# Kernel optimization log

Hardware: AMD Instinct MI355X
Metric: run time of the kernel (lower is better)

Reference implementation:

```python
import jax, jax.numpy as jnp
import numpy as np

H = 128        # hidden_channels
R = 32         # num_rbf
L = 2          # num_layers
CUTOFF = 4.5   # cutoff_upper (cutoff_lower = 0)
N_ATOMS = 2048
N_EDGES = 32768


def _tensor_norm(t):
    # Frobenius norm squared over the trailing 3x3 -> [N, H]
    return jnp.sum(t * t, axis=(-2, -1))


def _decompose(t):
    # Split into isotropic (I), antisymmetric (A), traceless symmetric (S) parts.
    eye = jnp.eye(3, dtype=t.dtype)
    I = (jnp.trace(t, axis1=-2, axis2=-1) / 3.0)[..., None, None] * eye
    A = 0.5 * (t - jnp.swapaxes(t, -2, -1))
    S = 0.5 * (t + jnp.swapaxes(t, -2, -1)) - I
    return I, A, S


def _chan_mix(T, W):
    # torch nn.Linear(H, H, bias=False) applied on the channel axis of [N,H,3,3]
    return jnp.einsum('nhij,gh->ngij', T, W)


def _interaction(X, edge_index, edge_weight, edge_attr, q,
                 W1, b1, W2, b2, W3, b3, Wt):
    N = X.shape[0]
    src, dst = edge_index[0], edge_index[1]
    # cosine cutoff (cutoff_lower = 0)
    C = 0.5 * (jnp.cos(edge_weight * (jnp.pi / CUTOFF)) + 1.0)
    C = C * (edge_weight < CUTOFF).astype(C.dtype)
    # edge scalar MLP: R -> H -> 2H -> 3H, silu
    ea = jax.nn.silu(edge_attr @ W1.T + b1)
    ea = jax.nn.silu(ea @ W2.T + b2)
    ea = jax.nn.silu(ea @ W3.T + b3)
    ea = (ea * C[:, None]).reshape(-1, H, 3)       # [E, H, 3]
    # normalize node tensors
    X = X / (_tensor_norm(X) + 1.0)[..., None, None]
    I, A, S = _decompose(X)
    I = _chan_mix(I, Wt[0])
    A = _chan_mix(A, Wt[1])
    S = _chan_mix(S, Wt[2])
    Y = I + A + S
    # per-edge tensor messages (Im + Am + Sm fused before the scatter)
    msg = (ea[:, :, 0, None, None] * I[dst]
           + ea[:, :, 1, None, None] * A[dst]
           + ea[:, :, 2, None, None] * S[dst])   # [E, H, 3, 3]
    M = jax.ops.segment_sum(msg, src, num_segments=N)
    # O(3) group: symmetrized tensor product, scaled by charge factor
    AB = jnp.matmul(M, Y) + jnp.matmul(Y, M)
    I, A, S = _decompose((1.0 + 0.1 * q[:, None, None, None]) * AB)
    normp1 = (_tensor_norm(I + A + S) + 1.0)[..., None, None]
    I, A, S = I / normp1, A / normp1, S / normp1
    I = _chan_mix(I, Wt[3])
    A = _chan_mix(A, Wt[4])
    S = _chan_mix(S, Wt[5])
    dX = I + A + S
    return X + dX + (1.0 + 0.1 * q[:, None, None, None]) * jnp.matmul(dX, dX)


def setup_inputs() -> dict:
    key = jax.random.key(0)
    ks = jax.random.split(key, 10)
    N, E = N_ATOMS, N_EDGES
    X = jax.random.normal(ks[0], (N, H, 3, 3), jnp.float32)
    edge_index = jax.random.randint(ks[1], (2, E), 0, N, jnp.int32)
    edge_weight = jax.random.uniform(ks[2], (E,), jnp.float32, 0.1, CUTOFF)
    edge_attr = jax.random.normal(ks[3], (E, R), jnp.float32)
    q = jax.random.normal(ks[4], (N,), jnp.float32) * 0.1
    s = 0.05
    Ws1 = jax.random.normal(ks[5], (L, H, R), jnp.float32) * s
    bs1 = jnp.zeros((L, H), jnp.float32)
    Ws2 = jax.random.normal(ks[6], (L, 2 * H, H), jnp.float32) * s
    bs2 = jnp.zeros((L, 2 * H), jnp.float32)
    Ws3 = jax.random.normal(ks[7], (L, 3 * H, 2 * H), jnp.float32) * s
    bs3 = jnp.zeros((L, 3 * H), jnp.float32)
    Wt = jax.random.normal(ks[8], (L, 6, H, H), jnp.float32) * s
    return dict(X=X, edge_attr=edge_attr, edge_weight=edge_weight, q=q,
                Ws1=Ws1, bs1=bs1, Ws2=Ws2, bs2=bs2, Ws3=Ws3, bs3=bs3,
                Wt=Wt, edge_index=edge_index)


def reference(X, edge_attr, edge_weight, q, Ws1, bs1, Ws2, bs2, Ws3, bs3, Wt, edge_index):
    for l in range(L):
        X = _interaction(X, edge_index, edge_weight, edge_attr, q,
                         Ws1[l], bs1[l], Ws2[l], bs2[l], Ws3[l], bs3[l], Wt[l])
    return X
```

## Files before the change

kernel.cpp:

```cpp
#include <hip/hip_runtime.h>
#include <hip/hip_bf16.h>
#include <math.h>

#define H 128
#define R 32
#define NATOMS 2048
#define NEDGES 32768
#define NH (NATOMS * H)
#define NP 1152
#define CUTOFF_F 4.5f
#define PI_OVER_CUTOFF 0.6981317007977318f

typedef __bf16 bf16x8 __attribute__((ext_vector_type(8)));
typedef float f32x4 __attribute__((ext_vector_type(4)));
typedef short short8 __attribute__((ext_vector_type(8)));
typedef unsigned short u16x4 __attribute__((ext_vector_type(4)));

#define BAR_LGKM() do { \
    asm volatile("s_waitcnt lgkmcnt(0)" ::: "memory"); \
    __builtin_amdgcn_s_barrier(); \
    asm volatile("" ::: "memory"); \
} while (0)

__device__ __forceinline__ float silu_f(float x) {
    return x / (1.f + __expf(-x));
}
__device__ __forceinline__ float b2f(unsigned short u) {
    return __uint_as_float(((unsigned)u) << 16);
}
__device__ __forceinline__ unsigned short f2b(float f) {
    __hip_bfloat16 h = __float2bfloat16(f);
    return __builtin_bit_cast(unsigned short, h);
}

__device__ __forceinline__ void build_full(const float d[9], float m[9]) {
    float i0 = d[0], a01 = d[1], a02 = d[2], a12 = d[3];
    float s00 = d[4], s01 = d[5], s02 = d[6], s11 = d[7], s12 = d[8];
    float s22 = -(s00 + s11);
    m[0] = i0 + s00;  m[1] = a01 + s01;  m[2] = a02 + s02;
    m[3] = s01 - a01; m[4] = i0 + s11;   m[5] = a12 + s12;
    m[6] = s02 - a02; m[7] = s12 - a12;  m[8] = i0 + s22;
}

#define C0 (NEDGES * R)
#define C1 (2 * H * R)
#define C2 (2 * 2 * H * H)
#define C3 (2 * 3 * H * 2 * H)
#define C4 (2 * 6 * H * H)
#define C5 2048
#define CAST_TOTAL (C0 + C1 + C2 + C3 + C4 + C5 + NH)
__global__ __launch_bounds__(256) void k_cast_all(
        const float* __restrict__ ea, const float* __restrict__ w1,
        const float* __restrict__ w2, const float* __restrict__ w3,
        const float* __restrict__ wt,
        __hip_bfloat16* __restrict__ oea, __hip_bfloat16* __restrict__ ow1,
        __hip_bfloat16* __restrict__ ow2, __hip_bfloat16* __restrict__ ow3,
        __hip_bfloat16* __restrict__ owt, int* __restrict__ cnt,
        const float* __restrict__ X, float* __restrict__ Xn,
        __hip_bfloat16* __restrict__ Db) {
    int i = blockIdx.x * 256 + threadIdx.x;
    if (i < C0) { oea[i] = __float2bfloat16(ea[i]); return; }
    i -= C0;
    if (i < C1) { ow1[i] = __float2bfloat16(w1[i]); return; }
    i -= C1;
    if (i < C2) { ow2[i] = __float2bfloat16(w2[i]); return; }
    i -= C2;
    if (i < C3) { ow3[i] = __float2bfloat16(w3[i]); return; }
    i -= C3;
    if (i < C4) { owt[i] = __float2bfloat16(wt[i]); return; }
    i -= C4;
    if (i < C5) { cnt[i] = 0; return; }
    i -= C5;
    if (i < NH) {
        const float* x = X + (size_t)i * 9;
        float v[9];
        float ss = 0.f;
#pragma unroll
        for (int j = 0; j < 9; j++) { v[j] = x[j]; ss += v[j] * v[j]; }
        float inv = 1.f / (ss + 1.f);
#pragma unroll
        for (int j = 0; j < 9; j++) { v[j] *= inv; Xn[(size_t)i * 9 + j] = v[j]; }
        float i0 = (v[0] + v[4] + v[8]) * (1.f / 3.f);
        unsigned short* D = (unsigned short*)Db + (size_t)(i >> 7) * NP + (i & 127);
        D[0 * H] = f2b(i0);
        D[1 * H] = f2b(0.5f * (v[1] - v[3]));
        D[2 * H] = f2b(0.5f * (v[2] - v[6]));
        D[3 * H] = f2b(0.5f * (v[5] - v[7]));
        D[4 * H] = f2b(v[0] - i0);
        D[5 * H] = f2b(0.5f * (v[1] + v[3]));
        D[6 * H] = f2b(0.5f * (v[2] + v[6]));
        D[7 * H] = f2b(v[4] - i0);
        D[8 * H] = f2b(0.5f * (v[5] + v[7]));
    }
}

struct TGm {
    static constexpr int BKm = 64;
    static constexpr int RB  = 128;
    static constexpr int SWZ = 7;
    static constexpr int NIT = 2;
    static constexpr int ABYTES = 128 * RB;
    static constexpr int BBYTES = 64 * RB;
    static constexpr int AISS = ABYTES / 4096;
    static constexpr int BISS = BBYTES / 4096;
    static constexpr int LDSB = ABYTES + BBYTES;
};

__device__ __forceinline__ void tile_gemm_mix(
        const __hip_bfloat16* __restrict__ A, int strideA,
        const __hip_bfloat16* __restrict__ W,
        int m0, int n0, char* lds, f32x4 acc[4][2]) {
    using T = TGm;
    const int t = threadIdx.x;
    const int lane = t & 63;
    const int w = t >> 6;

    auto stage = [&](int b, int it) {
        const int k0 = it * T::BKm;
        char* As = lds + b * T::LDSB;
        char* Bs = As + T::ABYTES;
#pragma unroll
        for (int i = 0; i < T::AISS; i++) {
            int base = (w * T::AISS + i) * 1024;
            int lin = base + lane * 16;
            int row = lin / T::RB;
            int slot = (lin % T::RB) >> 4;
            int sl = slot ^ (row & T::SWZ);
            const char* src = (const char*)(A + (size_t)(m0 + row) * strideA + k0) + sl * 16;
            __builtin_amdgcn_global_load_lds(
                (const __attribute__((address_space(1))) void*)src,
                (__attribute__((address_space(3))) void*)(As + base), 16, 0, 0);
        }
#pragma unroll
        for (int i = 0; i < T::BISS; i++) {
            int base = (w * T::BISS + i) * 1024;
            int lin = base + lane * 16;
            int row = lin / T::RB;
            int slot = (lin % T::RB) >> 4;
            int sl = slot ^ (row & T::SWZ);
            const char* src = (const char*)(W + (size_t)(n0 + row) * H + k0) + sl * 16;
            __builtin_amdgcn_global_load_lds(
                (const __attribute__((address_space(1))) void*)src,
                (__attribute__((address_space(3))) void*)(Bs + base), 16, 0, 0);
        }
    };

    auto compute = [&](int b) {
        const char* As = lds + b * T::LDSB;
        const char* Bs = As + T::ABYTES;
        const int wm = (w & 1) * 64;
        const int wn = (w >> 1) * 32;
        const int rA = wm + (lane & 15);
        const int rB = wn + (lane & 15);
        const int c = lane >> 4;
#pragma unroll
        for (int kk = 0; kk < T::BKm / 32; kk++) {
            bf16x8 av[4], bv[2];
#pragma unroll
            for (int mf = 0; mf < 4; mf++) {
                int row = rA + mf * 16;
                int sp = (kk * 4 + c) ^ (row & T::SWZ);
                av[mf] = __builtin_bit_cast(bf16x8,
                    *(const short8*)(As + row * T::RB + sp * 16));
            }
#pragma unroll
            for (int nf = 0; nf < 2; nf++) {
                int row = rB + nf * 16;
                int sp = (kk * 4 + c) ^ (row & T::SWZ);
                bv[nf] = __builtin_bit_cast(bf16x8,
                    *(const short8*)(Bs + row * T::RB + sp * 16));
            }
#pragma unroll
            for (int mf = 0; mf < 4; mf++)
#pragma unroll
                for (int nf = 0; nf < 2; nf++)
                    acc[mf][nf] = __builtin_amdgcn_mfma_f32_16x16x32_bf16(
                        av[mf], bv[nf], acc[mf][nf], 0, 0, 0);
        }
    };

    stage(0, 0);
    asm volatile("s_waitcnt vmcnt(0)" ::: "memory");
    __syncthreads();
    for (int it = 0; it < T::NIT; it++) {
        int b = it & 1;
        if (it + 1 < T::NIT) stage(b ^ 1, it + 1);
        compute(b);
        asm volatile("s_waitcnt vmcnt(0)" ::: "memory");
        __syncthreads();
    }
}

__global__ __launch_bounds__(256) void k_mix(
        const __hip_bfloat16* __restrict__ Db, const __hip_bfloat16* __restrict__ Wtb,
        __hip_bfloat16* __restrict__ Outp, int partOff) {
    __shared__ char lds[2 * TGm::LDSB];
    int c = blockIdx.z;
    int part = (c == 0) ? 0 : ((c < 4) ? 1 : 2);
    const __hip_bfloat16* A = Db + (size_t)c * H;
    const __hip_bfloat16* W = Wtb + (size_t)(partOff + part) * H * H;
    unsigned short* Out = (unsigned short*)Outp + (size_t)c * H;
    const int lane = threadIdx.x & 63;
    const int w = threadIdx.x >> 6;
    const int wm = (w & 1) * 64, wn = (w >> 1) * 32;
    const int m0 = blockIdx.x * 128, n0 = blockIdx.y * 64;
    f32x4 acc[4][2] = {};
    tile_gemm_mix(A, NP, W, m0, n0, lds, acc);
#pragma unroll
    for (int mf = 0; mf < 4; mf++)
#pragma unroll
        for (int r = 0; r < 4; r++) {
            int row = m0 + wm + mf * 16 + (lane >> 4) * 4 + r;
#pragma unroll
            for (int nf = 0; nf < 2; nf++) {
                int col = n0 + wn + nf * 16 + (lane & 15);
                Out[(size_t)row * NP + col] = f2b(acc[mf][nf][r]);
            }
        }
}

#define ETILE 64
#define PAD0 40
#define PAD1 136
#define PAD2 264
#define SA2_B (ETILE * PAD2 * 2)
#define SA1_B (ETILE * PAD1 * 2)
#define SEA_OFF SA1_B

__global__ __launch_bounds__(512, 4) void k_mlp_fused(
        const __hip_bfloat16* __restrict__ eaB,
        const __hip_bfloat16* __restrict__ W1b, const __hip_bfloat16* __restrict__ W2b,
        const __hip_bfloat16* __restrict__ W3b,
        const float* __restrict__ bs1, const float* __restrict__ bs2,
        const float* __restrict__ bs3, const float* __restrict__ ew,
        __hip_bfloat16* __restrict__ ea3g) {
    const int l = blockIdx.z;
    const unsigned short* W1 = (const unsigned short*)W1b + (size_t)l * (H * R);
    const unsigned short* W2 = (const unsigned short*)W2b + (size_t)l * (2 * H * H);
    const unsigned short* W3 = (const unsigned short*)W3b + (size_t)l * (3 * H * 2 * H);
    const float* b1 = bs1 + (size_t)l * H;
    const float* b2 = bs2 + (size_t)l * 2 * H;
    const float* b3 = bs3 + (size_t)l * 3 * H;
    unsigned short* outp = (unsigned short*)ea3g + (size_t)l * NEDGES * 384;
    const int e0 = blockIdx.x * ETILE;

    __shared__ char smem[SA2_B + ETILE * 4 + 16];
    unsigned short* sA2 = (unsigned short*)smem;
    unsigned short* sA1 = (unsigned short*)smem;
    unsigned short* sEA = (unsigned short*)(smem + SEA_OFF);
    float* sEW = (float*)(smem + SA2_B);

    const int t = threadIdx.x;
    const int lane = t & 63;
    const int w = t >> 6;
    const int q = lane >> 4;
    const int li = lane & 15;

    const int cbase1 = w * 16;
    const int cbase2 = w * 32;
    const int cbase3 = w * 48;

    bf16x8 av1 = __builtin_bit_cast(bf16x8,
        *(const short8*)(W1 + (size_t)(cbase1 + li) * R + q * 8));
    f32x4 bb1 = *(const f32x4*)&b1[cbase1 + q * 4];

    {
        if (t < 256) {
            int row = t >> 2, c8 = t & 3;
            *(uint4*)(sEA + row * PAD0 + c8 * 8) =
                *(const uint4*)((const unsigned short*)eaB + (size_t)(e0 + row) * R + c8 * 8);
        }
        if (t < ETILE) sEW[t] = ew[e0 + t];
    }
    BAR_LGKM();

    f32x4 acc1[4] = {};
#pragma unroll
    for (int ef = 0; ef < 4; ef++) {
        bf16x8 bv = __builtin_bit_cast(bf16x8,
            *(const short8*)(sEA + (ef * 16 + li) * PAD0 + q * 8));
        acc1[ef] = __builtin_amdgcn_mfma_f32_16x16x32_bf16(av1, bv, acc1[ef], 0, 0, 0);
    }

    bf16x8 a2[4][2];
#pragma unroll
    for (int ks = 0; ks < 4; ks++)
#pragma unroll
        for (int mf = 0; mf < 2; mf++)
            a2[ks][mf] = __builtin_bit_cast(bf16x8,
                *(const short8*)(W2 + (size_t)(cbase2 + mf * 16 + li) * H
                                 + ks * 32 + q * 8));
    f32x4 bb2[2];
#pragma unroll
    for (int mf = 0; mf < 2; mf++)
        bb2[mf] = *(const f32x4*)&b2[cbase2 + mf * 16 + q * 4];

#pragma unroll
    for (int ef = 0; ef < 4; ef++) {
        u16x4 o;
#pragma unroll
        for (int r = 0; r < 4; r++) o[r] = f2b(silu_f(acc1[ef][r] + bb1[r]));
        *(u16x4*)(sA1 + (ef * 16 + li) * PAD1 + cbase1 + q * 4) = o;
    }
    BAR_LGKM();

    f32x4 acc2[2][4] = {};
#pragma unroll
    for (int ks = 0; ks < 4; ks++) {
        bf16x8 bv[4];
#pragma unroll
        for (int ef = 0; ef < 4; ef++)
            bv[ef] = __builtin_bit_cast(bf16x8,
                *(const short8*)(sA1 + (ef * 16 + li) * PAD1 + ks * 32 + q * 8));
        __builtin_amdgcn_s_setprio(1);
#pragma unroll
        for (int mf = 0; mf < 2; mf++)
#pragma unroll
            for (int ef = 0; ef < 4; ef++)
                acc2[mf][ef] = __builtin_amdgcn_mfma_f32_16x16x32_bf16(
                    a2[ks][mf], bv[ef], acc2[mf][ef], 0, 0, 0);
        __builtin_amdgcn_s_setprio(0);
    }

    bf16x8 a3[3][3];
#pragma unroll
    for (int pk = 0; pk < 3; pk++)
#pragma unroll
        for (int mf = 0; mf < 3; mf++)
            a3[pk][mf] = __builtin_bit_cast(bf16x8,
                *(const short8*)(W3 + (size_t)(cbase3 + mf * 16 + li) * (2 * H)
                                 + pk * 32 + q * 8));

    BAR_LGKM();
#pragma unroll
    for (int mf = 0; mf < 2; mf++)
#pragma unroll
        for (int ef = 0; ef < 4; ef++) {
            u16x4 o;
#pragma unroll
            for (int r = 0; r < 4; r++)
                o[r] = f2b(silu_f(acc2[mf][ef][r] + bb2[mf][r]));
            *(u16x4*)(sA2 + (ef * 16 + li) * PAD2 + cbase2 + mf * 16 + q * 4) = o;
        }
    BAR_LGKM();

    f32x4 acc3[3][4] = {};
#pragma unroll
    for (int ks = 0; ks < 8; ks++) {
        const int slot = ks % 3;
        bf16x8 bv[4];
#pragma unroll
        for (int ef = 0; ef < 4; ef++)
            bv[ef] = __builtin_bit_cast(bf16x8,
                *(const short8*)(sA2 + (ef * 16 + li) * PAD2 + ks * 32 + q * 8));
        __builtin_amdgcn_s_setprio(1);
#pragma unroll
        for (int mf = 0; mf < 3; mf++)
#pragma unroll
            for (int ef = 0; ef < 4; ef++)
                acc3[mf][ef] = __builtin_amdgcn_mfma_f32_16x16x32_bf16(
                    a3[slot][mf], bv[ef], acc3[mf][ef], 0, 0, 0);
        __builtin_amdgcn_s_setprio(0);
        if (ks + 3 < 8) {
#pragma unroll
            for (int mf = 0; mf < 3; mf++)
                a3[slot][mf] = __builtin_bit_cast(bf16x8,
                    *(const short8*)(W3 + (size_t)(cbase3 + mf * 16 + li) * (2 * H)
                                     + (ks + 3) * 32 + q * 8));
        }
    }
    f32x4 bb3[3];
#pragma unroll
    for (int mf = 0; mf < 3; mf++)
        bb3[mf] = *(const f32x4*)&b3[cbase3 + mf * 16 + q * 4];
#pragma unroll
    for (int ef = 0; ef < 4; ef++) {
        int edge = ef * 16 + li;
        float wv = sEW[edge];
        float cs = (wv < CUTOFF_F) ? 0.5f * (__cosf(wv * PI_OVER_CUTOFF) + 1.f) : 0.f;
#pragma unroll
        for (int mf = 0; mf < 3; mf++) {
            u16x4 o;
#pragma unroll
            for (int r = 0; r < 4; r++)
                o[r] = f2b(silu_f(acc3[mf][ef][r] + bb3[mf][r]) * cs);
            *(u16x4*)(outp + (size_t)(e0 + edge) * 384 + cbase3 + mf * 16 + q * 4) = o;
        }
    }
}

__global__ __launch_bounds__(256) void k_hist(
        const int* __restrict__ eidx, int* __restrict__ cnt) {
    int e = blockIdx.x * 256 + threadIdx.x;
    if (e < NEDGES) atomicAdd(&cnt[eidx[e]], 1);
}

__global__ __launch_bounds__(256) void k_scan(
        const int* __restrict__ cnt, int* __restrict__ rowstart,
        int* __restrict__ cursor) {
    __shared__ int partial[256];
    int t = threadIdx.x;
    int loc[8];
    int run = 0;
#pragma unroll
    for (int j = 0; j < 8; j++) {
        int v = cnt[t * 8 + j];
        loc[j] = run; run += v;
    }
    partial[t] = run;
    __syncthreads();
    if (t == 0) {
        int acc = 0;
        for (int i = 0; i < 256; i++) { int v = partial[i]; partial[i] = acc; acc += v; }
        rowstart[2048] = acc;
    }
    __syncthreads();
    int base = partial[t];
#pragma unroll
    for (int j = 0; j < 8; j++) {
        rowstart[t * 8 + j] = base + loc[j];
        cursor[t * 8 + j] = base + loc[j];
    }
}

__global__ __launch_bounds__(256) void k_fill(
        const int* __restrict__ eidx, int* __restrict__ cursor,
        int* __restrict__ elist) {
    int e = blockIdx.x * 256 + threadIdx.x;
    if (e >= NEDGES) return;
    int src = eidx[e];
    int pos = atomicAdd(&cursor[src], 1);
    elist[pos] = e;
}

__global__ __launch_bounds__(256) void k_gather_ab(
        const __hip_bfloat16* __restrict__ ea ,
        const int* __restrict__ eidx,
        const int* __restrict__ rowstart, const int* __restrict__ elist,
        const __hip_bfloat16* __restrict__ Yb, const float* __restrict__ q,
        __hip_bfloat16* __restrict__ Tb) {
    int gid = blockIdx.x * 256 + threadIdx.x;
    int n = gid >> 7;
    int t7 = gid & 127;
    int hp = t7 >> 1;
    int half = t7 & 1;
    int h0 = hp << 1;
    int beg = rowstart[n], end = rowstart[n + 1];
    const unsigned short* Y = (const unsigned short*)Yb;

    int hcol = h0 + half;
    const unsigned short* ypn = Y + (size_t)n * NP + hcol;
    float yd[9];
#pragma unroll
    for (int c = 0; c < 9; c++) yd[c] = b2f(ypn[(size_t)c * H]);

    float acc[9][2];
#pragma unroll
    for (int c = 0; c < 9; c++) { acc[c][0] = 0.f; acc[c][1] = 0.f; }

    int idx = beg + half;
    int e = 0, dst = 0;
    if (idx < end) { e = elist[idx]; dst = eidx[NEDGES + e]; }
    while (idx < end) {
        int nidx = idx + 2;
        int ne = e, ndst = dst;
        if (nidx < end) { ne = elist[nidx]; ndst = eidx[NEDGES + ne]; }
        const unsigned short* eap = (const unsigned short*)ea + (size_t)e * 384 + h0 * 3;
        unsigned u0 = *(const unsigned*)(eap);
        unsigned u1 = *(const unsigned*)(eap + 2);
        unsigned u2 = *(const unsigned*)(eap + 4);
        float w0a = b2f(u0 & 0xffff), w1a = b2f(u0 >> 16);
        float w2a = b2f(u1 & 0xffff), w0b = b2f(u1 >> 16);
        float w1b = b2f(u2 & 0xffff), w2b = b2f(u2 >> 16);
        const unsigned short* yp = Y + (size_t)dst * NP + h0;
        ushort2 y;
        y = *(const ushort2*)(yp + 0 * H); acc[0][0] += w0a * b2f(y.x); acc[0][1] += w0b * b2f(y.y);
        y = *(const ushort2*)(yp + 1 * H); acc[1][0] += w1a * b2f(y.x); acc[1][1] += w1b * b2f(y.y);
        y = *(const ushort2*)(yp + 2 * H); acc[2][0] += w1a * b2f(y.x); acc[2][1] += w1b * b2f(y.y);
        y = *(const ushort2*)(yp + 3 * H); acc[3][0] += w1a * b2f(y.x); acc[3][1] += w1b * b2f(y.y);
#pragma unroll
        for (int c = 4; c < 9; c++) {
            y = *(const ushort2*)(yp + c * H);
            acc[c][0] += w2a * b2f(y.x); acc[c][1] += w2b * b2f(y.y);
        }
        idx = nidx; e = ne; dst = ndst;
    }
#pragma unroll
    for (int c = 0; c < 9; c++) {
        acc[c][0] += __shfl_xor(acc[c][0], 1);
        acc[c][1] += __shfl_xor(acc[c][1], 1);
    }
    float scale = 1.f + 0.1f * q[n];
    float md[9];
#pragma unroll
    for (int c = 0; c < 9; c++) md[c] = acc[c][half];
    float m[9], yf[9];
    build_full(md, m);
    build_full(yd, yf);
    float ab[9];
#pragma unroll
    for (int ii = 0; ii < 3; ii++)
#pragma unroll
        for (int jj = 0; jj < 3; jj++) {
            float s = 0.f;
#pragma unroll
            for (int kk = 0; kk < 3; kk++)
                s += m[ii * 3 + kk] * yf[kk * 3 + jj] + yf[ii * 3 + kk] * m[kk * 3 + jj];
            ab[ii * 3 + jj] = s;
        }
    float nrm = 0.f;
#pragma unroll
    for (int j = 0; j < 9; j++) { ab[j] *= scale; nrm += ab[j] * ab[j]; }
    float inv = 1.f / (nrm + 1.f);
    float tr3 = (ab[0] + ab[4] + ab[8]) * (1.f / 3.f);
    unsigned short* T = (unsigned short*)Tb + (size_t)n * NP + hcol;
    T[0 * H] = f2b(tr3 * inv);
    T[1 * H] = f2b(0.5f * (ab[1] - ab[3]) * inv);
    T[2 * H] = f2b(0.5f * (ab[2] - ab[6]) * inv);
    T[3 * H] = f2b(0.5f * (ab[5] - ab[7]) * inv);
    T[4 * H] = f2b((ab[0] - tr3) * inv);
    T[5 * H] = f2b(0.5f * (ab[1] + ab[3]) * inv);
    T[6 * H] = f2b(0.5f * (ab[2] + ab[6]) * inv);
    T[7 * H] = f2b((ab[4] - tr3) * inv);
    T[8 * H] = f2b(0.5f * (ab[5] + ab[7]) * inv);
}

template <bool PREP>
__global__ __launch_bounds__(256) void k_final(
        const __hip_bfloat16* __restrict__ dXb, const float* __restrict__ Xn,
        const float* __restrict__ q, float* __restrict__ Xout,
        float* __restrict__ XnW, __hip_bfloat16* __restrict__ Db) {
    int i = blockIdx.x * 256 + threadIdx.x;
    if (i >= NH) return;
    const unsigned short* dX = (const unsigned short*)dXb + (size_t)(i >> 7) * NP + (i & 127);
    float dd[9];
#pragma unroll
    for (int c = 0; c < 9; c++) dd[c] = b2f(dX[(size_t)c * H]);
    float dx[9];
    build_full(dd, dx);
    float scale = 1.f + 0.1f * q[i >> 7];
    float out[9];
#pragma unroll
    for (int ii = 0; ii < 3; ii++)
#pragma unroll
        for (int jj = 0; jj < 3; jj++) {
            float s = 0.f;
#pragma unroll
            for (int kk = 0; kk < 3; kk++)
                s += dx[ii * 3 + kk] * dx[kk * 3 + jj];
            out[ii * 3 + jj] = Xn[(size_t)i * 9 + ii * 3 + jj] + dx[ii * 3 + jj] + scale * s;
        }
#pragma unroll
    for (int j = 0; j < 9; j++) Xout[(size_t)i * 9 + j] = out[j];
    if (PREP) {
        float ss = 0.f;
#pragma unroll
        for (int j = 0; j < 9; j++) ss += out[j] * out[j];
        float inv = 1.f / (ss + 1.f);
        float v[9];
#pragma unroll
        for (int j = 0; j < 9; j++) { v[j] = out[j] * inv; XnW[(size_t)i * 9 + j] = v[j]; }
        float i0 = (v[0] + v[4] + v[8]) * (1.f / 3.f);
        unsigned short* D = (unsigned short*)Db + (size_t)(i >> 7) * NP + (i & 127);
        D[0 * H] = f2b(i0);
        D[1 * H] = f2b(0.5f * (v[1] - v[3]));
        D[2 * H] = f2b(0.5f * (v[2] - v[6]));
        D[3 * H] = f2b(0.5f * (v[5] - v[7]));
        D[4 * H] = f2b(v[0] - i0);
        D[5 * H] = f2b(0.5f * (v[1] + v[3]));
        D[6 * H] = f2b(0.5f * (v[2] + v[6]));
        D[7 * H] = f2b(v[4] - i0);
        D[8 * H] = f2b(0.5f * (v[5] + v[7]));
    }
}

extern "C" void kernel_launch(void* const* d_in, const int* in_sizes, int n_in,
                              void* d_out, int out_size, void* d_ws, size_t ws_size,
                              hipStream_t stream) {
    const float* X          = (const float*)d_in[0];
    const float* edge_attr  = (const float*)d_in[1];
    const float* edge_weight= (const float*)d_in[2];
    const float* q          = (const float*)d_in[3];
    const float* Ws1        = (const float*)d_in[4];
    const float* bs1        = (const float*)d_in[5];
    const float* Ws2        = (const float*)d_in[6];
    const float* bs2        = (const float*)d_in[7];
    const float* Ws3        = (const float*)d_in[8];
    const float* bs3        = (const float*)d_in[9];
    const float* Wt         = (const float*)d_in[10];
    const int*   eidx       = (const int*)d_in[11];
    float* Xout = (float*)d_out;

    char* p = (char*)d_ws;
    auto alloc = [&](size_t bytes) -> char* {
        char* r = p; p += (bytes + 255) & ~(size_t)255; return r;
    };
    size_t nodeBytes = (size_t)NH * 9 * sizeof(float);
    float* Xn   = (float*)alloc(nodeBytes);
    __hip_bfloat16* Db = (__hip_bfloat16*)alloc((size_t)NH * 9 * 2);
    __hip_bfloat16* Yb = (__hip_bfloat16*)alloc((size_t)NH * 9 * 2);
    __hip_bfloat16* eaB = (__hip_bfloat16*)alloc((size_t)C0 * 2);
    __hip_bfloat16* W1b = (__hip_bfloat16*)alloc((size_t)C1 * 2);
    __hip_bfloat16* W2b = (__hip_bfloat16*)alloc((size_t)C2 * 2);
    __hip_bfloat16* W3b = (__hip_bfloat16*)alloc((size_t)C3 * 2);
    __hip_bfloat16* Wtb = (__hip_bfloat16*)alloc((size_t)C4 * 2);
    __hip_bfloat16* ea3g = (__hip_bfloat16*)alloc((size_t)2 * NEDGES * 384 * 2);
    int* cnt      = (int*)alloc(2048 * 4);
    int* rowstart = (int*)alloc(2049 * 4);
    int* cursor   = (int*)alloc(2048 * 4);
    int* elist    = (int*)alloc(NEDGES * 4);

    k_cast_all<<<(CAST_TOTAL + 255) / 256, 256, 0, stream>>>(
        edge_attr, Ws1, Ws2, Ws3, Wt, eaB, W1b, W2b, W3b, Wtb, cnt,
        X, Xn, Db);

    k_hist<<<NEDGES / 256, 256, 0, stream>>>(eidx, cnt);
    k_scan<<<1, 256, 0, stream>>>(cnt, rowstart, cursor);
    k_fill<<<NEDGES / 256, 256, 0, stream>>>(eidx, cursor, elist);

    k_mlp_fused<<<dim3(NEDGES / ETILE, 1, 2), 512, 0, stream>>>(
        eaB, W1b, W2b, W3b, bs1, bs2, bs3, edge_weight, ea3g);

    for (int l = 0; l < 2; l++) {
        const __hip_bfloat16* Wtl = Wtb + (size_t)l * 6 * H * H;
        const __hip_bfloat16* ea3 = ea3g + (size_t)l * NEDGES * 384;

        k_mix<<<dim3(NATOMS / 128, 2, 9), 256, 0, stream>>>(Db, Wtl, Yb, 0);
        k_gather_ab<<<NH / 256, 256, 0, stream>>>(
            ea3, eidx, rowstart, elist, Yb, q, Db);
        k_mix<<<dim3(NATOMS / 128, 2, 9), 256, 0, stream>>>(Db, Wtl, Yb, 3);
        if (l == 0)
            k_final<true><<<NH / 256, 256, 0, stream>>>(Yb, Xn, q, Xout, Xn, Db);
        else
            k_final<false><<<NH / 256, 256, 0, stream>>>(Yb, Xn, q, Xout, nullptr, nullptr);
    }
}
```

Before: 158.4 us.

## Interleave Y components per channel pair for vector gathers, use four lanes per pair

The first k_mix now writes Y in a layout where the 9 components of each channel pair sit contiguously (24 halves, padded row stride). k_gather_ab can then fetch a neighbour's data with two 16-byte loads and one 4-byte load instead of nine scattered 4-byte loads. It also splits each channel pair's edge list across four lanes instead of two, doubling the thread count and reducing with an extra shuffle stage. The s_setprio hints are removed from the edge MLP kernel. The padded layout spends more memory, and half of the lanes sit idle in the epilogue.

```diff
diff --git a/kernel.cpp b/kernel.cpp
--- a/kernel.cpp
+++ b/kernel.cpp
@@ -8,6 +8,7 @@
 #define NEDGES 32768
 #define NH (NATOMS * H)
 #define NP 1152
+#define NPY 1536
 #define CUTOFF_F 4.5f
 #define PI_OVER_CUTOFF 0.6981317007977318f
 
@@ -27,6 +28,12 @@
 }
 __device__ __forceinline__ float b2f(unsigned short u) {
     return __uint_as_float(((unsigned)u) << 16);
+}
+__device__ __forceinline__ float b2f_lo(unsigned u) {
+    return __uint_as_float(u << 16);
+}
+__device__ __forceinline__ float b2f_hi(unsigned u) {
+    return __uint_as_float(u & 0xffff0000u);
 }
 __device__ __forceinline__ unsigned short f2b(float f) {
     __hip_bfloat16 h = __float2bfloat16(f);
@@ -191,6 +198,7 @@
     }
 }
 
+template <int LAYOUT>
 __global__ __launch_bounds__(256) void k_mix(
         const __hip_bfloat16* __restrict__ Db, const __hip_bfloat16* __restrict__ Wtb,
         __hip_bfloat16* __restrict__ Outp, int partOff) {
@@ -199,7 +207,7 @@
     int part = (c == 0) ? 0 : ((c < 4) ? 1 : 2);
     const __hip_bfloat16* A = Db + (size_t)c * H;
     const __hip_bfloat16* W = Wtb + (size_t)(partOff + part) * H * H;
-    unsigned short* Out = (unsigned short*)Outp + (size_t)c * H;
+    unsigned short* O = (unsigned short*)Outp;
     const int lane = threadIdx.x & 63;
     const int w = threadIdx.x >> 6;
     const int wm = (w & 1) * 64, wn = (w >> 1) * 32;
@@ -214,7 +222,11 @@
 #pragma unroll
             for (int nf = 0; nf < 2; nf++) {
                 int col = n0 + wn + nf * 16 + (lane & 15);
-                Out[(size_t)row * NP + col] = f2b(acc[mf][nf][r]);
+                if (LAYOUT == 0)
+                    O[(size_t)row * NP + (size_t)c * H + col] = f2b(acc[mf][nf][r]);
+                else
+                    O[(size_t)row * NPY + (col >> 1) * 24 + c * 2 + (col & 1)] =
+                        f2b(acc[mf][nf][r]);
             }
         }
 }
@@ -312,14 +324,12 @@
         for (int ef = 0; ef < 4; ef++)
             bv[ef] = __builtin_bit_cast(bf16x8,
                 *(const short8*)(sA1 + (ef * 16 + li) * PAD1 + ks * 32 + q * 8));
-        __builtin_amdgcn_s_setprio(1);
 #pragma unroll
         for (int mf = 0; mf < 2; mf++)
 #pragma unroll
             for (int ef = 0; ef < 4; ef++)
                 acc2[mf][ef] = __builtin_amdgcn_mfma_f32_16x16x32_bf16(
                     a2[ks][mf], bv[ef], acc2[mf][ef], 0, 0, 0);
-        __builtin_amdgcn_s_setprio(0);
     }
 
     bf16x8 a3[3][3];
@@ -353,14 +363,12 @@
         for (int ef = 0; ef < 4; ef++)
             bv[ef] = __builtin_bit_cast(bf16x8,
                 *(const short8*)(sA2 + (ef * 16 + li) * PAD2 + ks * 32 + q * 8));
-        __builtin_amdgcn_s_setprio(1);
 #pragma unroll
         for (int mf = 0; mf < 3; mf++)
 #pragma unroll
             for (int ef = 0; ef < 4; ef++)
                 acc3[mf][ef] = __builtin_amdgcn_mfma_f32_16x16x32_bf16(
                     a3[slot][mf], bv[ef], acc3[mf][ef], 0, 0, 0);
-        __builtin_amdgcn_s_setprio(0);
         if (ks + 3 < 8) {
 #pragma unroll
             for (int mf = 0; mf < 3; mf++)
@@ -437,63 +445,68 @@
         const __hip_bfloat16* __restrict__ ea ,
         const int* __restrict__ eidx,
         const int* __restrict__ rowstart, const int* __restrict__ elist,
-        const __hip_bfloat16* __restrict__ Yb, const float* __restrict__ q,
-        __hip_bfloat16* __restrict__ Tb) {
+        const __hip_bfloat16* __restrict__ Yb ,
+        const float* __restrict__ q,
+        __hip_bfloat16* __restrict__ Tb ) {
     int gid = blockIdx.x * 256 + threadIdx.x;
-    int n = gid >> 7;
-    int t7 = gid & 127;
-    int hp = t7 >> 1;
-    int half = t7 & 1;
+    int n = gid >> 8;
+    int t8 = gid & 255;
+    int hp = t8 >> 2;
+    int quarter = t8 & 3;
     int h0 = hp << 1;
     int beg = rowstart[n], end = rowstart[n + 1];
     const unsigned short* Y = (const unsigned short*)Yb;
 
-    int hcol = h0 + half;
-    const unsigned short* ypn = Y + (size_t)n * NP + hcol;
-    float yd[9];
-#pragma unroll
-    for (int c = 0; c < 9; c++) yd[c] = b2f(ypn[(size_t)c * H]);
-
     float acc[9][2];
 #pragma unroll
     for (int c = 0; c < 9; c++) { acc[c][0] = 0.f; acc[c][1] = 0.f; }
 
-    int idx = beg + half;
+    int idx = beg + quarter;
     int e = 0, dst = 0;
     if (idx < end) { e = elist[idx]; dst = eidx[NEDGES + e]; }
     while (idx < end) {
-        int nidx = idx + 2;
+        int nidx = idx + 4;
         int ne = e, ndst = dst;
         if (nidx < end) { ne = elist[nidx]; ndst = eidx[NEDGES + ne]; }
         const unsigned short* eap = (const unsigned short*)ea + (size_t)e * 384 + h0 * 3;
         unsigned u0 = *(const unsigned*)(eap);
         unsigned u1 = *(const unsigned*)(eap + 2);
         unsigned u2 = *(const unsigned*)(eap + 4);
-        float w0a = b2f(u0 & 0xffff), w1a = b2f(u0 >> 16);
-        float w2a = b2f(u1 & 0xffff), w0b = b2f(u1 >> 16);
-        float w1b = b2f(u2 & 0xffff), w2b = b2f(u2 >> 16);
-        const unsigned short* yp = Y + (size_t)dst * NP + h0;
-        ushort2 y;
-        y = *(const ushort2*)(yp + 0 * H); acc[0][0] += w0a * b2f(y.x); acc[0][1] += w0b * b2f(y.y);
-        y = *(const ushort2*)(yp + 1 * H); acc[1][0] += w1a * b2f(y.x); acc[1][1] += w1b * b2f(y.y);
-        y = *(const ushort2*)(yp + 2 * H); acc[2][0] += w1a * b2f(y.x); acc[2][1] += w1b * b2f(y.y);
-        y = *(const ushort2*)(yp + 3 * H); acc[3][0] += w1a * b2f(y.x); acc[3][1] += w1b * b2f(y.y);
-#pragma unroll
-        for (int c = 4; c < 9; c++) {
-            y = *(const ushort2*)(yp + c * H);
-            acc[c][0] += w2a * b2f(y.x); acc[c][1] += w2b * b2f(y.y);
-        }
+        float w0a = b2f_lo(u0), w1a = b2f_hi(u0);
+        float w2a = b2f_lo(u1), w0b = b2f_hi(u1);
+        float w1b = b2f_lo(u2), w2b = b2f_hi(u2);
+        const unsigned short* yr = Y + (size_t)dst * NPY + hp * 24;
+        uint4 ya = *(const uint4*)yr;
+        uint4 yb = *(const uint4*)(yr + 8);
+        unsigned yc = *(const unsigned*)(yr + 16);
+        acc[0][0] += w0a * b2f_lo(ya.x); acc[0][1] += w0b * b2f_hi(ya.x);
+        acc[1][0] += w1a * b2f_lo(ya.y); acc[1][1] += w1b * b2f_hi(ya.y);
+        acc[2][0] += w1a * b2f_lo(ya.z); acc[2][1] += w1b * b2f_hi(ya.z);
+        acc[3][0] += w1a * b2f_lo(ya.w); acc[3][1] += w1b * b2f_hi(ya.w);
+        acc[4][0] += w2a * b2f_lo(yb.x); acc[4][1] += w2b * b2f_hi(yb.x);
+        acc[5][0] += w2a * b2f_lo(yb.y); acc[5][1] += w2b * b2f_hi(yb.y);
+        acc[6][0] += w2a * b2f_lo(yb.z); acc[6][1] += w2b * b2f_hi(yb.z);
+        acc[7][0] += w2a * b2f_lo(yb.w); acc[7][1] += w2b * b2f_hi(yb.w);
+        acc[8][0] += w2a * b2f_lo(yc);   acc[8][1] += w2b * b2f_hi(yc);
         idx = nidx; e = ne; dst = ndst;
     }
 #pragma unroll
     for (int c = 0; c < 9; c++) {
         acc[c][0] += __shfl_xor(acc[c][0], 1);
         acc[c][1] += __shfl_xor(acc[c][1], 1);
-    }
+        acc[c][0] += __shfl_xor(acc[c][0], 2);
+        acc[c][1] += __shfl_xor(acc[c][1], 2);
+    }
+    if (quarter >= 2) return;
+    int hcol = h0 + quarter;
+    const unsigned short* yr = Y + (size_t)n * NPY + hp * 24;
     float scale = 1.f + 0.1f * q[n];
-    float md[9];
-#pragma unroll
-    for (int c = 0; c < 9; c++) md[c] = acc[c][half];
+    float md[9], yd[9];
+#pragma unroll
+    for (int c = 0; c < 9; c++) {
+        md[c] = acc[c][quarter];
+        yd[c] = b2f(yr[c * 2 + quarter]);
+    }
     float m[9], yf[9];
     build_full(md, m);
     build_full(yd, yf);
@@ -598,7 +611,7 @@
     size_t nodeBytes = (size_t)NH * 9 * sizeof(float);
     float* Xn   = (float*)alloc(nodeBytes);
     __hip_bfloat16* Db = (__hip_bfloat16*)alloc((size_t)NH * 9 * 2);
-    __hip_bfloat16* Yb = (__hip_bfloat16*)alloc((size_t)NH * 9 * 2);
+    __hip_bfloat16* Yb = (__hip_bfloat16*)alloc((size_t)NATOMS * NPY * 2);
     __hip_bfloat16* eaB = (__hip_bfloat16*)alloc((size_t)C0 * 2);
     __hip_bfloat16* W1b = (__hip_bfloat16*)alloc((size_t)C1 * 2);
     __hip_bfloat16* W2b = (__hip_bfloat16*)alloc((size_t)C2 * 2);
@@ -625,10 +638,10 @@
         const __hip_bfloat16* Wtl = Wtb + (size_t)l * 6 * H * H;
         const __hip_bfloat16* ea3 = ea3g + (size_t)l * NEDGES * 384;
 
-        k_mix<<<dim3(NATOMS / 128, 2, 9), 256, 0, stream>>>(Db, Wtl, Yb, 0);
-        k_gather_ab<<<NH / 256, 256, 0, stream>>>(
+        k_mix<1><<<dim3(NATOMS / 128, 2, 9), 256, 0, stream>>>(Db, Wtl, Yb, 0);
+        k_gather_ab<<<(NH * 2) / 256, 256, 0, stream>>>(
             ea3, eidx, rowstart, elist, Yb, q, Db);
-        k_mix<<<dim3(NATOMS / 128, 2, 9), 256, 0, stream>>>(Db, Wtl, Yb, 3);
+        k_mix<0><<<dim3(NATOMS / 128, 2, 9), 256, 0, stream>>>(Db, Wtl, Yb, 3);
         if (l == 0)
             k_final<true><<<NH / 256, 256, 0, stream>>>(Yb, Xn, q, Xout, Xn, Db);
         else
```

After: 170.2 us. +7.4%, slower.
